# Kernel tuning notes

Hardware: AMD Instinct MI355X
Metric: run time of the kernel (lower is better)

The kernel has to match this reference:

```python
import jax, jax.numpy as jnp
import numpy as np

N = 100000
E = 640000
ND = 128   # node_dim
ED = 128   # edge_dim
HD = 256   # hidden_dim
EPS = 1e-5


def _mlp_ln(x, W1, b1, W2, b2, W3, b3, g, beta):
    h = jax.nn.relu(x @ W1 + b1)
    h = jax.nn.relu(h @ W2 + b2)
    o = h @ W3 + b3
    mu = jnp.mean(o, axis=-1, keepdims=True)
    var = jnp.mean(jnp.square(o - mu), axis=-1, keepdims=True)
    return (o - mu) * jax.lax.rsqrt(var + EPS) * g + beta


def setup_inputs() -> dict:
    key = jax.random.key(0)
    ks = jax.random.split(key, 20)
    s = 0.02
    inp = {
        "node_emb": jax.random.normal(ks[0], (N, ND), jnp.float32),
        "edge_emb": jax.random.normal(ks[1], (E, ED), jnp.float32),
        "src": jax.random.randint(ks[2], (E,), 0, N),
        "dst": jax.random.randint(ks[3], (E,), 0, N),
        "num_nodes": N,
        # edge MLP: in = 2*ND + ED
        "eW1": jax.random.normal(ks[4], (2 * ND + ED, HD), jnp.float32) * s,
        "eb1": jnp.zeros((HD,), jnp.float32),
        "eW2": jax.random.normal(ks[5], (HD, HD), jnp.float32) * s,
        "eb2": jnp.zeros((HD,), jnp.float32),
        "eW3": jax.random.normal(ks[6], (HD, ED), jnp.float32) * s,
        "eb3": jnp.zeros((ED,), jnp.float32),
        "eg": jnp.ones((ED,), jnp.float32),
        "ebeta": jnp.zeros((ED,), jnp.float32),
        # node MLP: in = ND + ED
        "nW1": jax.random.normal(ks[7], (ND + ED, HD), jnp.float32) * s,
        "nb1": jnp.zeros((HD,), jnp.float32),
        "nW2": jax.random.normal(ks[8], (HD, HD), jnp.float32) * s,
        "nb2": jnp.zeros((HD,), jnp.float32),
        "nW3": jax.random.normal(ks[9], (HD, ND), jnp.float32) * s,
        "nb3": jnp.zeros((ND,), jnp.float32),
        "ng": jnp.ones((ND,), jnp.float32),
        "nbeta": jnp.zeros((ND,), jnp.float32),
    }
    return inp


def reference(node_emb, edge_emb, src, dst, num_nodes,
              eW1, eb1, eW2, eb2, eW3, eb3, eg, ebeta,
              nW1, nb1, nW2, nb2, nW3, nb3, ng, nbeta):
    # Edge update: e' = MLP(concat(h_i, h_j, e)) + e
    edge_input = jnp.concatenate([node_emb[src], node_emb[dst], edge_emb], axis=-1)
    edge_emb_new = _mlp_ln(edge_input, eW1, eb1, eW2, eb2, eW3, eb3, eg, ebeta) + edge_emb
    # Mean aggregation over incoming edges per dst node
    agg = jax.ops.segment_sum(edge_emb_new, dst, num_segments=num_nodes)
    count = jax.ops.segment_sum(jnp.ones((dst.shape[0], 1), node_emb.dtype), dst, num_segments=num_nodes)
    agg = agg / jnp.maximum(count, 1.0)
    # Node update: h' = MLP(concat(h, agg)) + h
    node_input = jnp.concatenate([node_emb, agg], axis=-1)
    node_emb_new = _mlp_ln(node_input, nW1, nb1, nW2, nb2, nW3, nb3, ng, nbeta) + node_emb
    return (node_emb_new, edge_emb_new)
```

## Files before the change

### kernel.cpp

```cpp
#include <hip/hip_runtime.h>
#include <hip/hip_bf16.h>

typedef __attribute__((ext_vector_type(8))) short bf16x8;
typedef __attribute__((ext_vector_type(4))) short s16x4;
typedef __attribute__((ext_vector_type(4))) float f32x4;

__device__ __forceinline__ short f2bf(float f) {
  union { __hip_bfloat16 h; short s; } u;
  u.h = __float2bfloat16(f);
  return u.s;
}

__device__ __forceinline__ void gld_lds16(const short* g, short* l) {
  __builtin_amdgcn_global_load_lds((const __attribute__((address_space(1))) unsigned*)g,
                                   (__attribute__((address_space(3))) unsigned*)l,
                                   16, 0, 0);
}

#define BARX(N) asm volatile("s_waitcnt vmcnt(" #N ") lgkmcnt(0)\ns_barrier" ::: "memory")
#define BARLG() asm volatile("s_waitcnt lgkmcnt(0)\ns_barrier" ::: "memory")

template <bool PERM>
__global__ void prep_kernel(const float* __restrict__ W, short* __restrict__ out, int K, int N) {
  int s = blockIdx.x * 256 + threadIdx.x;
  int NF = N >> 4;
  int total = (K >> 5) * NF * 64;
  if (s >= total) return;
  int l = s & 63, kcf = s >> 6;
  int kc = kcf / NF, f = kcf - kc * NF;
  int kg = l >> 4, l16 = l & 15;
  bf16x8 o;
#pragma unroll
  for (int e = 0; e < 8; ++e) {
    int kh = kc * 32 + kg * 8 + e;
    int k = PERM ? ((kh & ~63) | ((kh & 3) << 4) | ((kh >> 2) & 15)) : kh;
    o[e] = f2bf(W[(size_t)k * N + f * 16 + l16]);
  }
  *(bf16x8*)(out + (size_t)s * 8) = o;
}

__global__ void count_kernel(const int* __restrict__ dst, int* __restrict__ cnt, int E) {
  int i = blockIdx.x * 256 + threadIdx.x;
  if (i < E) atomicAdd(&cnt[dst[i]], 1);
}

__global__ __launch_bounds__(1024) void scan_kernel(const int* __restrict__ cnt,
                                                    int* __restrict__ off,
                                                    int* __restrict__ cursor, int N) {
  __shared__ int wsum[16];
  const int t = threadIdx.x;
  const int w = t >> 6, l = t & 63;
  int running = 0;
  for (int base = 0; base < N; base += 1024) {
    int i = base + t;
    int v = (i < N) ? cnt[i] : 0;
    int x = v;
#pragma unroll
    for (int d = 1; d < 64; d <<= 1) { int y = __shfl_up(x, d); if (l >= d) x += y; }
    if (l == 63) wsum[w] = x;
    __syncthreads();
    if (w == 0) {
      int s = (l < 16) ? wsum[l] : 0;
#pragma unroll
      for (int d = 1; d < 16; d <<= 1) { int y = __shfl_up(s, d); if (l >= d) s += y; }
      if (l < 16) wsum[l] = s;
    }
    __syncthreads();
    int total = wsum[15];
    int wo = (w > 0) ? wsum[w - 1] : 0;
    int excl = running + wo + x - v;
    if (i < N) { off[i] = excl; cursor[i] = excl; }
    running += total;
    __syncthreads();
  }
  if (t == 0) off[N] = running;
}

__global__ void scatter_kernel(const int* __restrict__ dst, int* __restrict__ cursor,
                               int* __restrict__ eidx, int E) {
  int e = blockIdx.x * 256 + threadIdx.x;
  if (e < E) {
    int p = atomicAdd(&cursor[dst[e]], 1);
    eidx[p] = e;
  }
}

__global__ void agg_kernel(const float* __restrict__ edge_out, const int* __restrict__ eidx,
                           const int* __restrict__ off, float* __restrict__ agg, int N) {
  int n = blockIdx.x * 4 + (threadIdx.x >> 6);
  if (n >= N) return;
  int l = threadIdx.x & 63;
  int beg = off[n], end = off[n + 1];
  float ax = 0.f, ay = 0.f;
  int i = beg;
  for (; i + 4 <= end; i += 4) {
    int e0 = eidx[i], e1 = eidx[i + 1], e2 = eidx[i + 2], e3 = eidx[i + 3];
    float2 v0 = *(const float2*)(edge_out + (size_t)e0 * 128 + l * 2);
    float2 v1 = *(const float2*)(edge_out + (size_t)e1 * 128 + l * 2);
    float2 v2 = *(const float2*)(edge_out + (size_t)e2 * 128 + l * 2);
    float2 v3 = *(const float2*)(edge_out + (size_t)e3 * 128 + l * 2);
    ax += v0.x + v1.x + v2.x + v3.x;
    ay += v0.y + v1.y + v2.y + v3.y;
  }
  for (; i < end; ++i) {
    int e = eidx[i];
    float2 v = *(const float2*)(edge_out + (size_t)e * 128 + l * 2);
    ax += v.x; ay += v.y;
  }
  float inv = 1.0f / fmaxf((float)(end - beg), 1.0f);
  *(float2*)(agg + (size_t)n * 128 + l * 2) = make_float2(ax * inv, ay * inv);
}

struct F8 { float4 a, b; };

template <bool IS_EDGE>
__launch_bounds__(512, 2)
__global__ void mlp_kernel(const float* __restrict__ node_emb, const float* __restrict__ edge_emb,
                           const int* __restrict__ src, const int* __restrict__ dst,
                           const short* __restrict__ wAll,
                           const float* __restrict__ b1, const float* __restrict__ b2,
                           const float* __restrict__ b3,
                           const float* __restrict__ gam, const float* __restrict__ bet,
                           const float* __restrict__ agg,
                           float* __restrict__ out_base, int M) {
  extern __shared__ short smem[];
  short* BsBase = smem;
  short* AsBase = smem + 24576;
  short* Hs     = smem + 32768;

  const int tid = threadIdx.x;
  const int m0 = blockIdx.x * 128;
  const int w = tid >> 6, lane = tid & 63, l16 = lane & 15, kg = lane >> 4;
  const int wr = w >> 2, wc = w & 3;

  constexpr int NC1 = IS_EDGE ? 12 : 8;

  const int grow = tid >> 2;
  const int gk = tid & 3;
  const int grc = min(m0 + grow, M - 1);
  const int aslot = (grow >> 4) * 64 + gk * 16 + (grow & 15);
  int gsr = 0, gdr = 0;
  if (IS_EDGE) { gsr = src[grc]; gdr = dst[grc]; }

  float b1v[4], b2v[4];
#pragma unroll
  for (int ct = 0; ct < 4; ++ct) {
    int col = wc * 64 + ct * 16 + l16;
    b1v[ct] = b1[col];
    b2v[ct] = b2[col];
  }
  float b3v[8], gv[8], bev[8];
#pragma unroll
  for (int f = 0; f < 8; ++f) {
    int col = f * 16 + l16;
    b3v[f] = b3[col]; gv[f] = gam[col]; bev[f] = bet[col];
  }

  f32x4 acc[16];
#pragma unroll
  for (int i = 0; i < 16; ++i) { f32x4 z = {0.f, 0.f, 0.f, 0.f}; acc[i] = z; }

  auto bsbuf = [&](int v) -> short* { return BsBase + (size_t)(v % 3) * 8192; };
  auto stage1024 = [&](int v) {
    const short* g = wAll + (size_t)v * 8192;
    short* l = bsbuf(v);
    gld_lds16(g + (size_t)tid * 8, l + (size_t)tid * 8);
    gld_lds16(g + (size_t)(512 + tid) * 8, l + (size_t)(512 + tid) * 8);
  };

  auto gatherA = [&](int c) -> F8 {
    const float* q;
    if (IS_EDGE) {
      if (c < 4)      q = node_emb + (size_t)gsr * 128 + c * 32 + gk * 8;
      else if (c < 8) q = node_emb + (size_t)gdr * 128 + (c - 4) * 32 + gk * 8;
      else            q = edge_emb + (size_t)grc * 128 + (c - 8) * 32 + gk * 8;
    } else {
      if (c < 4) q = node_emb + (size_t)grc * 128 + c * 32 + gk * 8;
      else       q = agg + (size_t)grc * 128 + (c - 4) * 32 + gk * 8;
    }
    F8 r;
    r.a = *(const float4*)q;
    r.b = *(const float4*)(q + 4);
    return r;
  };
  auto writeA = [&](const F8& p, int buf) {
    float t[8];
    *(float4*)t = p.a; *(float4*)(t + 4) = p.b;
    bf16x8 o;
#pragma unroll
    for (int e = 0; e < 8; ++e) o[e] = f2bf(t[e]);
    *(bf16x8*)&AsBase[(size_t)buf * 4096 + (size_t)aslot * 8] = o;
  };

  auto mfma16 = [&](bf16x8* a, bf16x8* b) {
#pragma unroll
    for (int rt = 0; rt < 4; ++rt)
#pragma unroll
      for (int ct = 0; ct < 4; ++ct)
        acc[rt * 4 + ct] = __builtin_amdgcn_mfma_f32_16x16x32_bf16(a[rt], b[ct], acc[rt * 4 + ct], 0, 0, 0);
  };

  auto compA = [&](int i) {
    const short* Ap = AsBase + (size_t)(i & 1) * 4096;
    const short* Bp = bsbuf(i);
    bf16x8 a[4], b[4];
#pragma unroll
    for (int rt = 0; rt < 4; ++rt)
      a[rt] = *(const bf16x8*)&Ap[(size_t)((wr * 4 + rt) * 64 + kg * 16 + l16) * 8];
#pragma unroll
    for (int ct = 0; ct < 4; ++ct)
      b[ct] = *(const bf16x8*)&Bp[(size_t)((wc * 4 + ct) * 64 + lane) * 8];
    mfma16(a, b);
  };

  auto computeH = [&](int j, const short* Bp) {
    bf16x8 a[4], b[4];
#pragma unroll
    for (int rt = 0; rt < 4; ++rt) {
      int row = wr * 64 + rt * 16 + l16;
      int ch = (j * 32 + kg * 8) ^ ((row & 7) << 3);
      a[rt] = *(const bf16x8*)&Hs[(size_t)row * 256 + ch];
    }
#pragma unroll
    for (int ct = 0; ct < 4; ++ct)
      b[ct] = *(const bf16x8*)&Bp[(size_t)((wc * 4 + ct) * 64 + lane) * 8];
    mfma16(a, b);
  };

  auto writeH = [&](const float* bv) {
#pragma unroll
    for (int rt = 0; rt < 4; ++rt)
#pragma unroll
      for (int q = 0; q < 4; ++q) {
        int row = wr * 64 + rt * 16 + kg * 4 + q;
        s16x4 v;
#pragma unroll
        for (int ct = 0; ct < 4; ++ct)
          v[ct] = f2bf(fmaxf(acc[rt * 4 + ct][q] + bv[ct], 0.f));
        int ch = (wc * 64 + l16 * 4) ^ ((row & 7) << 3);
        *(s16x4*)&Hs[(size_t)row * 256 + ch] = v;
      }
#pragma unroll
    for (int i = 0; i < 16; ++i) { f32x4 z = {0.f, 0.f, 0.f, 0.f}; acc[i] = z; }
  };

  auto computeL3 = [&](int kk, const short* Bp) {
    int row = w * 16 + l16;
    int ch = (kk * 32 + kg * 8) ^ ((row & 7) << 3);
    bf16x8 a = *(const bf16x8*)&Hs[(size_t)row * 256 + ch];
    const short* Bsub = Bp + (size_t)(kk & 1) * 4096;
#pragma unroll
    for (int f = 0; f < 8; ++f) {
      bf16x8 b = *(const bf16x8*)&Bsub[(size_t)(f * 64 + lane) * 8];
      acc[f] = __builtin_amdgcn_mfma_f32_16x16x32_bf16(a, b, acc[f], 0, 0, 0);
    }
  };

  F8 hold0 = gatherA(0);
  stage1024(0);
  stage1024(1);
  F8 hold = gatherA(1);
  writeA(hold0, 0);
  BARX(4);

#pragma unroll
  for (int i = 0; i < NC1; ++i) {
    stage1024(i + 2);
    F8 gnew = hold;
    if (i + 2 < NC1) gnew = gatherA(i + 2);
    compA(i);
    if (i + 1 < NC1) writeA(hold, (i + 1) & 1);
    if (i + 2 < NC1) { BARX(4); } else { BARX(2); }
    hold = gnew;
  }
  writeH(b1v);
  BARLG();

#pragma unroll
  for (int j = 0; j < 8; ++j) {
    int p = NC1 + j;
    stage1024(p + 2);
    computeH(j, bsbuf(p));
    BARX(2);
  }
  writeH(b2v);
  BARLG();

#pragma unroll
  for (int k = 0; k < 4; ++k) {
    int p = NC1 + 8 + k;
    if (k < 2) stage1024(p + 2);
    computeL3(2 * k, bsbuf(p));
    computeL3(2 * k + 1, bsbuf(p));
    if (k == 0 || k == 1) { BARX(2); }
    else if (k == 2)      { BARX(0); }
  }

#pragma unroll
  for (int q = 0; q < 4; ++q) {
    int rg = m0 + w * 16 + kg * 4 + q;
    float o[8], s1 = 0.f, s2 = 0.f;
#pragma unroll
    for (int f = 0; f < 8; ++f) {
      float x = acc[f][q] + b3v[f];
      o[f] = x; s1 += x; s2 += x * x;
    }
#pragma unroll
    for (int m = 1; m <= 8; m <<= 1) { s1 += __shfl_xor(s1, m); s2 += __shfl_xor(s2, m); }
    float mu = s1 * (1.f / 128.f);
    float var = s2 * (1.f / 128.f) - mu * mu;
    float rs = rsqrtf(var + 1e-5f);
    if (rg < M) {
      const float* resid = (IS_EDGE ? edge_emb : node_emb) + (size_t)rg * 128;
      float* op = out_base + (size_t)rg * 128;
#pragma unroll
      for (int f = 0; f < 8; ++f) {
        int col = f * 16 + l16;
        op[col] = (o[f] - mu) * rs * gv[f] + bev[f] + resid[col];
      }
    }
  }
}

extern "C" void kernel_launch(void* const* d_in, const int* in_sizes, int n_in,
                              void* d_out, int out_size, void* d_ws, size_t ws_size,
                              hipStream_t stream) {
  const float* node_emb = (const float*)d_in[0];
  const float* edge_emb = (const float*)d_in[1];
  const int*   src      = (const int*)d_in[2];
  const int*   dst      = (const int*)d_in[3];
  const float* eW1 = (const float*)d_in[5];
  const float* eb1 = (const float*)d_in[6];
  const float* eW2 = (const float*)d_in[7];
  const float* eb2 = (const float*)d_in[8];
  const float* eW3 = (const float*)d_in[9];
  const float* eb3 = (const float*)d_in[10];
  const float* eg  = (const float*)d_in[11];
  const float* ebt = (const float*)d_in[12];
  const float* nW1 = (const float*)d_in[13];
  const float* nb1 = (const float*)d_in[14];
  const float* nW2 = (const float*)d_in[15];
  const float* nb2 = (const float*)d_in[16];
  const float* nW3 = (const float*)d_in[17];
  const float* nb3 = (const float*)d_in[18];
  const float* ng  = (const float*)d_in[19];
  const float* nbt = (const float*)d_in[20];

  const int Nn = in_sizes[0] / 128;
  const int Ee = in_sizes[2];

  char* ws = (char*)d_ws;
  float* agg  = (float*)ws;  ws += (size_t)Nn * 128 * 4;
  int* cnt_i  = (int*)ws;    ws += (size_t)Nn * 4;
  int* cursor = (int*)ws;    ws += (size_t)Nn * 4;
  int* offv   = (int*)ws;    ws += (size_t)(Nn + 1) * 4;
  int* eidx   = (int*)ws;    ws += (size_t)Ee * 4;
  ws = (char*)(((uintptr_t)ws + 15) & ~(uintptr_t)15);
  short* wp = (short*)ws;
  short* eAll = wp;
  short* nAll = wp + 196608;

  float* out_node = (float*)d_out;
  float* out_edge = out_node + (size_t)Nn * 128;

  hipMemsetAsync(cnt_i, 0, (size_t)Nn * 4, stream);

  prep_kernel<false><<<48, 256, 0, stream>>>(eW1, eAll, 384, 256);
  prep_kernel<true><<<32, 256, 0, stream>>>(eW2, eAll + 98304, 256, 256);
  prep_kernel<true><<<16, 256, 0, stream>>>(eW3, eAll + 163840, 256, 128);
  prep_kernel<false><<<32, 256, 0, stream>>>(nW1, nAll, 256, 256);
  prep_kernel<true><<<32, 256, 0, stream>>>(nW2, nAll + 65536, 256, 256);
  prep_kernel<true><<<16, 256, 0, stream>>>(nW3, nAll + 131072, 256, 128);

  count_kernel<<<(Ee + 255) / 256, 256, 0, stream>>>(dst, cnt_i, Ee);
  scan_kernel<<<1, 1024, 0, stream>>>(cnt_i, offv, cursor, Nn);
  scatter_kernel<<<(Ee + 255) / 256, 256, 0, stream>>>(dst, cursor, eidx, Ee);

  mlp_kernel<true><<<(Ee + 127) / 128, 512, 131072, stream>>>(
      node_emb, edge_emb, src, dst, eAll,
      eb1, eb2, eb3, eg, ebt, agg, out_edge, Ee);

  agg_kernel<<<(Nn + 3) / 4, 256, 0, stream>>>(out_edge, eidx, offv, agg, Nn);

  mlp_kernel<false><<<(Nn + 127) / 128, 512, 131072, stream>>>(
      node_emb, edge_emb, src, dst, nAll,
      nb1, nb2, nb3, ng, nbt, agg, out_node, Nn);
}
```

Baseline: 751.8 us.

## Shrink MLP tiles to 64 rows with 256 threads and double-buffered weights

Reworks the fused MLP kernel from 128-row tiles with 8 waves and triple-buffered weight stages to 64-row tiles with 4 waves and double-buffered weight stages. Each wave now covers all 64 rows and a 64-column slice, shared memory per block drops from 128KB to 72KB, and wait counts are adjusted to fit the new pipeline depth. It also raises wave priority around MFMA bursts and adds scheduling barriers. The aim is more resident blocks and better latency hiding, but weight tiles are reused across half as many rows, so weight loads from L2 double and the shallower prefetch may expose more latency.

```diff
diff --git a/kernel.cpp b/kernel.cpp
--- a/kernel.cpp
+++ b/kernel.cpp
@@ -18,7 +18,6 @@
 }
 
 #define BARX(N) asm volatile("s_waitcnt vmcnt(" #N ") lgkmcnt(0)\ns_barrier" ::: "memory")
-#define BARLG() asm volatile("s_waitcnt lgkmcnt(0)\ns_barrier" ::: "memory")
 
 template <bool PERM>
 __global__ void prep_kernel(const float* __restrict__ W, short* __restrict__ out, int K, int N) {
@@ -114,7 +113,7 @@
 struct F8 { float4 a, b; };
 
 template <bool IS_EDGE>
-__launch_bounds__(512, 2)
+__launch_bounds__(256, 2)
 __global__ void mlp_kernel(const float* __restrict__ node_emb, const float* __restrict__ edge_emb,
                            const int* __restrict__ src, const int* __restrict__ dst,
                            const short* __restrict__ wAll,
@@ -124,14 +123,13 @@
                            const float* __restrict__ agg,
                            float* __restrict__ out_base, int M) {
   extern __shared__ short smem[];
-  short* BsBase = smem;
-  short* AsBase = smem + 24576;
-  short* Hs     = smem + 32768;
+  short* Bs = smem;
+  short* As = smem + 16384;
+  short* Hs = smem + 20480;
 
   const int tid = threadIdx.x;
-  const int m0 = blockIdx.x * 128;
+  const int m0 = blockIdx.x * 64;
   const int w = tid >> 6, lane = tid & 63, l16 = lane & 15, kg = lane >> 4;
-  const int wr = w >> 2, wc = w & 3;
 
   constexpr int NC1 = IS_EDGE ? 12 : 8;
 
@@ -145,7 +143,7 @@
   float b1v[4], b2v[4];
 #pragma unroll
   for (int ct = 0; ct < 4; ++ct) {
-    int col = wc * 64 + ct * 16 + l16;
+    int col = w * 64 + ct * 16 + l16;
     b1v[ct] = b1[col];
     b2v[ct] = b2[col];
   }
@@ -160,12 +158,12 @@
 #pragma unroll
   for (int i = 0; i < 16; ++i) { f32x4 z = {0.f, 0.f, 0.f, 0.f}; acc[i] = z; }
 
-  auto bsbuf = [&](int v) -> short* { return BsBase + (size_t)(v % 3) * 8192; };
-  auto stage1024 = [&](int v) {
+  auto stageU = [&](int v) {
     const short* g = wAll + (size_t)v * 8192;
-    short* l = bsbuf(v);
-    gld_lds16(g + (size_t)tid * 8, l + (size_t)tid * 8);
-    gld_lds16(g + (size_t)(512 + tid) * 8, l + (size_t)(512 + tid) * 8);
+    short* l = Bs + (size_t)(v & 1) * 8192;
+#pragma unroll
+    for (int s0 = 0; s0 < 4; ++s0)
+      gld_lds16(g + (size_t)(s0 * 256 + tid) * 8, l + (size_t)(s0 * 256 + tid) * 8);
   };
 
   auto gatherA = [&](int c) -> F8 {
@@ -189,27 +187,29 @@
     bf16x8 o;
 #pragma unroll
     for (int e = 0; e < 8; ++e) o[e] = f2bf(t[e]);
-    *(bf16x8*)&AsBase[(size_t)buf * 4096 + (size_t)aslot * 8] = o;
+    *(bf16x8*)&As[(size_t)buf * 2048 + (size_t)aslot * 8] = o;
   };
 
   auto mfma16 = [&](bf16x8* a, bf16x8* b) {
+    __builtin_amdgcn_s_setprio(1);
 #pragma unroll
     for (int rt = 0; rt < 4; ++rt)
 #pragma unroll
       for (int ct = 0; ct < 4; ++ct)
         acc[rt * 4 + ct] = __builtin_amdgcn_mfma_f32_16x16x32_bf16(a[rt], b[ct], acc[rt * 4 + ct], 0, 0, 0);
+    __builtin_amdgcn_s_setprio(0);
   };
 
   auto compA = [&](int i) {
-    const short* Ap = AsBase + (size_t)(i & 1) * 4096;
-    const short* Bp = bsbuf(i);
+    const short* Ap = As + (size_t)(i & 1) * 2048;
+    const short* Bp = Bs + (size_t)(i & 1) * 8192;
     bf16x8 a[4], b[4];
 #pragma unroll
     for (int rt = 0; rt < 4; ++rt)
-      a[rt] = *(const bf16x8*)&Ap[(size_t)((wr * 4 + rt) * 64 + kg * 16 + l16) * 8];
+      a[rt] = *(const bf16x8*)&Ap[(size_t)(rt * 64 + kg * 16 + l16) * 8];
 #pragma unroll
     for (int ct = 0; ct < 4; ++ct)
-      b[ct] = *(const bf16x8*)&Bp[(size_t)((wc * 4 + ct) * 64 + lane) * 8];
+      b[ct] = *(const bf16x8*)&Bp[(size_t)((w * 4 + ct) * 64 + lane) * 8];
     mfma16(a, b);
   };
 
@@ -217,13 +217,13 @@
     bf16x8 a[4], b[4];
 #pragma unroll
     for (int rt = 0; rt < 4; ++rt) {
-      int row = wr * 64 + rt * 16 + l16;
+      int row = rt * 16 + l16;
       int ch = (j * 32 + kg * 8) ^ ((row & 7) << 3);
       a[rt] = *(const bf16x8*)&Hs[(size_t)row * 256 + ch];
     }
 #pragma unroll
     for (int ct = 0; ct < 4; ++ct)
-      b[ct] = *(const bf16x8*)&Bp[(size_t)((wc * 4 + ct) * 64 + lane) * 8];
+      b[ct] = *(const bf16x8*)&Bp[(size_t)((w * 4 + ct) * 64 + lane) * 8];
     mfma16(a, b);
   };
 
@@ -232,12 +232,12 @@
     for (int rt = 0; rt < 4; ++rt)
 #pragma unroll
       for (int q = 0; q < 4; ++q) {
-        int row = wr * 64 + rt * 16 + kg * 4 + q;
+        int row = rt * 16 + kg * 4 + q;
         s16x4 v;
 #pragma unroll
         for (int ct = 0; ct < 4; ++ct)
           v[ct] = f2bf(fmaxf(acc[rt * 4 + ct][q] + bv[ct], 0.f));
-        int ch = (wc * 64 + l16 * 4) ^ ((row & 7) << 3);
+        int ch = (w * 64 + l16 * 4) ^ ((row & 7) << 3);
         *(s16x4*)&Hs[(size_t)row * 256 + ch] = v;
       }
 #pragma unroll
@@ -249,51 +249,60 @@
     int ch = (kk * 32 + kg * 8) ^ ((row & 7) << 3);
     bf16x8 a = *(const bf16x8*)&Hs[(size_t)row * 256 + ch];
     const short* Bsub = Bp + (size_t)(kk & 1) * 4096;
+    __builtin_amdgcn_s_setprio(1);
 #pragma unroll
     for (int f = 0; f < 8; ++f) {
       bf16x8 b = *(const bf16x8*)&Bsub[(size_t)(f * 64 + lane) * 8];
       acc[f] = __builtin_amdgcn_mfma_f32_16x16x32_bf16(a, b, acc[f], 0, 0, 0);
     }
-  };
-
-  F8 hold0 = gatherA(0);
-  stage1024(0);
-  stage1024(1);
+    __builtin_amdgcn_s_setprio(0);
+  };
+
+  F8 h0 = gatherA(0);
+  stageU(0);
+  __builtin_amdgcn_sched_barrier(0);
   F8 hold = gatherA(1);
-  writeA(hold0, 0);
-  BARX(4);
+  writeA(h0, 0);
+  __builtin_amdgcn_sched_barrier(0);
+  BARX(2);
 
 #pragma unroll
   for (int i = 0; i < NC1; ++i) {
-    stage1024(i + 2);
+    stageU(i + 1);
+    __builtin_amdgcn_sched_barrier(0);
     F8 gnew = hold;
     if (i + 2 < NC1) gnew = gatherA(i + 2);
+    __builtin_amdgcn_sched_barrier(0);
     compA(i);
     if (i + 1 < NC1) writeA(hold, (i + 1) & 1);
-    if (i + 2 < NC1) { BARX(4); } else { BARX(2); }
+    __builtin_amdgcn_sched_barrier(0);
+    if (i + 2 < NC1)      { BARX(2); }
+    else if (i + 1 < NC1) { BARX(0); }
+    else                  { BARX(4); }
     hold = gnew;
   }
   writeH(b1v);
-  BARLG();
+  BARX(0);
 
 #pragma unroll
   for (int j = 0; j < 8; ++j) {
-    int p = NC1 + j;
-    stage1024(p + 2);
-    computeH(j, bsbuf(p));
-    BARX(2);
+    int u = NC1 + j;
+    stageU(u + 1);
+    computeH(j, Bs + (size_t)(u & 1) * 8192);
+    if (j < 7) { BARX(0); }
+    else       { BARX(4); }
   }
   writeH(b2v);
-  BARLG();
+  BARX(0);
 
 #pragma unroll
   for (int k = 0; k < 4; ++k) {
-    int p = NC1 + 8 + k;
-    if (k < 2) stage1024(p + 2);
-    computeL3(2 * k, bsbuf(p));
-    computeL3(2 * k + 1, bsbuf(p));
-    if (k == 0 || k == 1) { BARX(2); }
-    else if (k == 2)      { BARX(0); }
+    int u = NC1 + 8 + k;
+    if (k < 3) stageU(u + 1);
+    const short* Bp = Bs + (size_t)(u & 1) * 8192;
+    computeL3(2 * k, Bp);
+    computeL3(2 * k + 1, Bp);
+    if (k < 3) { BARX(0); }
   }
 
 #pragma unroll
@@ -376,13 +385,13 @@
   scan_kernel<<<1, 1024, 0, stream>>>(cnt_i, offv, cursor, Nn);
   scatter_kernel<<<(Ee + 255) / 256, 256, 0, stream>>>(dst, cursor, eidx, Ee);
 
-  mlp_kernel<true><<<(Ee + 127) / 128, 512, 131072, stream>>>(
+  mlp_kernel<true><<<(Ee + 63) / 64, 256, 73728, stream>>>(
       node_emb, edge_emb, src, dst, eAll,
       eb1, eb2, eb3, eg, ebt, agg, out_edge, Ee);
 
   agg_kernel<<<(Nn + 3) / 4, 256, 0, stream>>>(out_edge, eidx, offv, agg, Nn);
 
-  mlp_kernel<false><<<(Nn + 127) / 128, 512, 131072, stream>>>(
+  mlp_kernel<false><<<(Nn + 63) / 64, 256, 73728, stream>>>(
       node_emb, edge_emb, src, dst, nAll,
       nb1, nb2, nb3, ng, nbt, agg, out_node, Nn);
 }
```

After: 778.3 us. 1.04x slower.

## Use 1024-thread MLP blocks with smaller per-wave tiles and unified pipeline loop

Applied to the files above, without the earlier changes.

Doubles the MLP kernel block to 16 waves, halving each wave's accumulator tile (2x4 MFMA tiles instead of 4x4) so more waves can hide latency. All three GEMM stages run in one unrolled loop over weight chunks with a single staged load per thread, with sched_barriers and adjusted vmcnt waits. The layer-3 output is split across two column halves, so the LayerNorm statistics are combined through a shared-memory partial-sum buffer and an extra block barrier. B-fragment LDS reads per MFMA go up, and the larger block may lower the number of resident blocks.

```diff
diff --git a/kernel.cpp b/kernel.cpp
--- a/kernel.cpp
+++ b/kernel.cpp
@@ -18,7 +18,6 @@
 }
 
 #define BARX(N) asm volatile("s_waitcnt vmcnt(" #N ") lgkmcnt(0)\ns_barrier" ::: "memory")
-#define BARLG() asm volatile("s_waitcnt lgkmcnt(0)\ns_barrier" ::: "memory")
 
 template <bool PERM>
 __global__ void prep_kernel(const float* __restrict__ W, short* __restrict__ out, int K, int N) {
@@ -111,10 +110,8 @@
   *(float2*)(agg + (size_t)n * 128 + l * 2) = make_float2(ax * inv, ay * inv);
 }
 
-struct F8 { float4 a, b; };
-
 template <bool IS_EDGE>
-__launch_bounds__(512, 2)
+__launch_bounds__(1024, 4)
 __global__ void mlp_kernel(const float* __restrict__ node_emb, const float* __restrict__ edge_emb,
                            const int* __restrict__ src, const int* __restrict__ dst,
                            const short* __restrict__ wAll,
@@ -124,21 +121,24 @@
                            const float* __restrict__ agg,
                            float* __restrict__ out_base, int M) {
   extern __shared__ short smem[];
-  short* BsBase = smem;
-  short* AsBase = smem + 24576;
-  short* Hs     = smem + 32768;
+  short* Bs = smem;
+  short* As = smem + 24576;
+  short* Hs = smem + 32768;
+  float2* pbuf = (float2*)(smem + 24576);
 
   const int tid = threadIdx.x;
   const int m0 = blockIdx.x * 128;
   const int w = tid >> 6, lane = tid & 63, l16 = lane & 15, kg = lane >> 4;
   const int wr = w >> 2, wc = w & 3;
+  const int r8 = w & 7, c2 = w >> 3;
 
   constexpr int NC1 = IS_EDGE ? 12 : 8;
-
-  const int grow = tid >> 2;
-  const int gk = tid & 3;
-  const int grc = min(m0 + grow, M - 1);
-  const int aslot = (grow >> 4) * 64 + gk * 16 + (grow & 15);
+  constexpr int NU = NC1 + 8 + 4;
+
+  const int gr = tid >> 3;
+  const int gq = tid & 7;
+  const int grc = min(m0 + gr, M - 1);
+  const int aoff = ((gr >> 4) * 64 + (gq >> 1) * 16 + (gr & 15)) * 8 + (gq & 1) * 4;
   int gsr = 0, gdr = 0;
   if (IS_EDGE) { gsr = src[grc]; gdr = dst[grc]; }
 
@@ -149,90 +149,76 @@
     b1v[ct] = b1[col];
     b2v[ct] = b2[col];
   }
-  float b3v[8], gv[8], bev[8];
-#pragma unroll
-  for (int f = 0; f < 8; ++f) {
-    int col = f * 16 + l16;
-    b3v[f] = b3[col]; gv[f] = gam[col]; bev[f] = bet[col];
-  }
-
-  f32x4 acc[16];
-#pragma unroll
-  for (int i = 0; i < 16; ++i) { f32x4 z = {0.f, 0.f, 0.f, 0.f}; acc[i] = z; }
-
-  auto bsbuf = [&](int v) -> short* { return BsBase + (size_t)(v % 3) * 8192; };
-  auto stage1024 = [&](int v) {
+
+  f32x4 acc[8];
+#pragma unroll
+  for (int i = 0; i < 8; ++i) { f32x4 z = {0.f, 0.f, 0.f, 0.f}; acc[i] = z; }
+
+  auto stageU = [&](int v) {
     const short* g = wAll + (size_t)v * 8192;
-    short* l = bsbuf(v);
+    short* l = Bs + (size_t)(v % 3) * 8192;
     gld_lds16(g + (size_t)tid * 8, l + (size_t)tid * 8);
-    gld_lds16(g + (size_t)(512 + tid) * 8, l + (size_t)(512 + tid) * 8);
-  };
-
-  auto gatherA = [&](int c) -> F8 {
+  };
+
+  auto gatherA = [&](int c) -> float4 {
+    int co = (c & 3) * 32 + gq * 4;
     const float* q;
     if (IS_EDGE) {
-      if (c < 4)      q = node_emb + (size_t)gsr * 128 + c * 32 + gk * 8;
-      else if (c < 8) q = node_emb + (size_t)gdr * 128 + (c - 4) * 32 + gk * 8;
-      else            q = edge_emb + (size_t)grc * 128 + (c - 8) * 32 + gk * 8;
+      if (c < 4)      q = node_emb + (size_t)gsr * 128 + co;
+      else if (c < 8) q = node_emb + (size_t)gdr * 128 + co;
+      else            q = edge_emb + (size_t)grc * 128 + co;
     } else {
-      if (c < 4) q = node_emb + (size_t)grc * 128 + c * 32 + gk * 8;
-      else       q = agg + (size_t)grc * 128 + (c - 4) * 32 + gk * 8;
-    }
-    F8 r;
-    r.a = *(const float4*)q;
-    r.b = *(const float4*)(q + 4);
-    return r;
-  };
-  auto writeA = [&](const F8& p, int buf) {
-    float t[8];
-    *(float4*)t = p.a; *(float4*)(t + 4) = p.b;
-    bf16x8 o;
-#pragma unroll
-    for (int e = 0; e < 8; ++e) o[e] = f2bf(t[e]);
-    *(bf16x8*)&AsBase[(size_t)buf * 4096 + (size_t)aslot * 8] = o;
-  };
-
-  auto mfma16 = [&](bf16x8* a, bf16x8* b) {
-#pragma unroll
-    for (int rt = 0; rt < 4; ++rt)
+      q = ((c < 4) ? node_emb : agg) + (size_t)grc * 128 + co;
+    }
+    return *(const float4*)q;
+  };
+  auto writeA = [&](float4 p, int buf) {
+    s16x4 o;
+    o[0] = f2bf(p.x); o[1] = f2bf(p.y); o[2] = f2bf(p.z); o[3] = f2bf(p.w);
+    *(s16x4*)&As[(size_t)buf * 4096 + aoff] = o;
+  };
+
+  auto compA = [&](int u) {
+    const short* Ap = As + (size_t)(u & 1) * 4096;
+    const short* Bp = Bs + (size_t)(u % 3) * 8192;
+    bf16x8 a[2], b[4];
+#pragma unroll
+    for (int rt = 0; rt < 2; ++rt)
+      a[rt] = *(const bf16x8*)&Ap[(size_t)((wr * 2 + rt) * 64 + kg * 16 + l16) * 8];
+#pragma unroll
+    for (int ct = 0; ct < 4; ++ct)
+      b[ct] = *(const bf16x8*)&Bp[(size_t)((wc * 4 + ct) * 64 + lane) * 8];
+#pragma unroll
+    for (int rt = 0; rt < 2; ++rt)
 #pragma unroll
       for (int ct = 0; ct < 4; ++ct)
         acc[rt * 4 + ct] = __builtin_amdgcn_mfma_f32_16x16x32_bf16(a[rt], b[ct], acc[rt * 4 + ct], 0, 0, 0);
   };
 
-  auto compA = [&](int i) {
-    const short* Ap = AsBase + (size_t)(i & 1) * 4096;
-    const short* Bp = bsbuf(i);
-    bf16x8 a[4], b[4];
-#pragma unroll
-    for (int rt = 0; rt < 4; ++rt)
-      a[rt] = *(const bf16x8*)&Ap[(size_t)((wr * 4 + rt) * 64 + kg * 16 + l16) * 8];
+  auto computeH = [&](int j, const short* Bp) {
+    bf16x8 a[2], b[4];
+#pragma unroll
+    for (int rt = 0; rt < 2; ++rt) {
+      int row = wr * 32 + rt * 16 + l16;
+      int ch = (j * 32 + kg * 8) ^ ((row & 7) << 3);
+      a[rt] = *(const bf16x8*)&Hs[(size_t)row * 256 + ch];
+    }
 #pragma unroll
     for (int ct = 0; ct < 4; ++ct)
       b[ct] = *(const bf16x8*)&Bp[(size_t)((wc * 4 + ct) * 64 + lane) * 8];
-    mfma16(a, b);
-  };
-
-  auto computeH = [&](int j, const short* Bp) {
-    bf16x8 a[4], b[4];
-#pragma unroll
-    for (int rt = 0; rt < 4; ++rt) {
-      int row = wr * 64 + rt * 16 + l16;
-      int ch = (j * 32 + kg * 8) ^ ((row & 7) << 3);
-      a[rt] = *(const bf16x8*)&Hs[(size_t)row * 256 + ch];
-    }
-#pragma unroll
-    for (int ct = 0; ct < 4; ++ct)
-      b[ct] = *(const bf16x8*)&Bp[(size_t)((wc * 4 + ct) * 64 + lane) * 8];
-    mfma16(a, b);
+#pragma unroll
+    for (int rt = 0; rt < 2; ++rt)
+#pragma unroll
+      for (int ct = 0; ct < 4; ++ct)
+        acc[rt * 4 + ct] = __builtin_amdgcn_mfma_f32_16x16x32_bf16(a[rt], b[ct], acc[rt * 4 + ct], 0, 0, 0);
   };
 
   auto writeH = [&](const float* bv) {
 #pragma unroll
-    for (int rt = 0; rt < 4; ++rt)
+    for (int rt = 0; rt < 2; ++rt)
 #pragma unroll
       for (int q = 0; q < 4; ++q) {
-        int row = wr * 64 + rt * 16 + kg * 4 + q;
+        int row = wr * 32 + rt * 16 + kg * 4 + q;
         s16x4 v;
 #pragma unroll
         for (int ct = 0; ct < 4; ++ct)
@@ -241,82 +227,96 @@
         *(s16x4*)&Hs[(size_t)row * 256 + ch] = v;
       }
 #pragma unroll
-    for (int i = 0; i < 16; ++i) { f32x4 z = {0.f, 0.f, 0.f, 0.f}; acc[i] = z; }
+    for (int i = 0; i < 8; ++i) { f32x4 z = {0.f, 0.f, 0.f, 0.f}; acc[i] = z; }
   };
 
   auto computeL3 = [&](int kk, const short* Bp) {
-    int row = w * 16 + l16;
+    int row = r8 * 16 + l16;
     int ch = (kk * 32 + kg * 8) ^ ((row & 7) << 3);
     bf16x8 a = *(const bf16x8*)&Hs[(size_t)row * 256 + ch];
     const short* Bsub = Bp + (size_t)(kk & 1) * 4096;
 #pragma unroll
-    for (int f = 0; f < 8; ++f) {
-      bf16x8 b = *(const bf16x8*)&Bsub[(size_t)(f * 64 + lane) * 8];
+    for (int f = 0; f < 4; ++f) {
+      bf16x8 b = *(const bf16x8*)&Bsub[(size_t)((c2 * 4 + f) * 64 + lane) * 8];
       acc[f] = __builtin_amdgcn_mfma_f32_16x16x32_bf16(a, b, acc[f], 0, 0, 0);
     }
   };
 
-  F8 hold0 = gatherA(0);
-  stage1024(0);
-  stage1024(1);
-  F8 hold = gatherA(1);
-  writeA(hold0, 0);
-  BARX(4);
-
-#pragma unroll
-  for (int i = 0; i < NC1; ++i) {
-    stage1024(i + 2);
-    F8 gnew = hold;
-    if (i + 2 < NC1) gnew = gatherA(i + 2);
-    compA(i);
-    if (i + 1 < NC1) writeA(hold, (i + 1) & 1);
-    if (i + 2 < NC1) { BARX(4); } else { BARX(2); }
-    hold = gnew;
-  }
-  writeH(b1v);
-  BARLG();
-
-#pragma unroll
-  for (int j = 0; j < 8; ++j) {
-    int p = NC1 + j;
-    stage1024(p + 2);
-    computeH(j, bsbuf(p));
-    BARX(2);
-  }
-  writeH(b2v);
-  BARLG();
-
-#pragma unroll
-  for (int k = 0; k < 4; ++k) {
-    int p = NC1 + 8 + k;
-    if (k < 2) stage1024(p + 2);
-    computeL3(2 * k, bsbuf(p));
-    computeL3(2 * k + 1, bsbuf(p));
-    if (k == 0 || k == 1) { BARX(2); }
-    else if (k == 2)      { BARX(0); }
-  }
-
+  float4 g0 = gatherA(0);
+  float4 ghold = gatherA(1);
+  stageU(0);
+  stageU(1);
+  writeA(g0, 0);
+  BARX(1);
+
+#pragma unroll
+  for (int u = 0; u < NU; ++u) {
+    if (u + 2 < NU) stageU(u + 2);
+    float4 gnew;
+    if (u + 2 < NC1) gnew = gatherA(u + 2);
+    __builtin_amdgcn_sched_barrier(0);
+
+    if (u < NC1) {
+      compA(u);
+    } else if (u < NC1 + 8) {
+      computeH(u - NC1, Bs + (size_t)(u % 3) * 8192);
+    } else {
+      const short* Bp = Bs + (size_t)(u % 3) * 8192;
+      computeL3(2 * (u - NC1 - 8), Bp);
+      computeL3(2 * (u - NC1 - 8) + 1, Bp);
+    }
+    if (u + 1 < NC1) writeA(ghold, (u + 1) & 1);
+    if (u == NC1 - 1) writeH(b1v);
+    if (u == NC1 + 7) {
+      asm volatile("s_waitcnt lgkmcnt(0)\ns_barrier" ::: "memory");
+      writeH(b2v);
+    }
+    __builtin_amdgcn_sched_barrier(0);
+
+    if (u + 2 < NC1)      { BARX(2); }
+    else if (u + 2 < NU)  { BARX(1); }
+    else if (u + 1 < NU)  { BARX(0); }
+    if (u + 2 < NC1) ghold = gnew;
+  }
+
+  float b3v[4], gv[4], bev[4];
+#pragma unroll
+  for (int f = 0; f < 4; ++f) {
+    int col = c2 * 64 + f * 16 + l16;
+    b3v[f] = b3[col]; gv[f] = gam[col]; bev[f] = bet[col];
+  }
 #pragma unroll
   for (int q = 0; q < 4; ++q) {
-    int rg = m0 + w * 16 + kg * 4 + q;
-    float o[8], s1 = 0.f, s2 = 0.f;
-#pragma unroll
-    for (int f = 0; f < 8; ++f) {
+    int row = r8 * 16 + kg * 4 + q;
+    float s1 = 0.f, s2 = 0.f;
+#pragma unroll
+    for (int f = 0; f < 4; ++f) {
       float x = acc[f][q] + b3v[f];
-      o[f] = x; s1 += x; s2 += x * x;
+      acc[f][q] = x;
+      s1 += x; s2 += x * x;
     }
 #pragma unroll
     for (int m = 1; m <= 8; m <<= 1) { s1 += __shfl_xor(s1, m); s2 += __shfl_xor(s2, m); }
-    float mu = s1 * (1.f / 128.f);
-    float var = s2 * (1.f / 128.f) - mu * mu;
+    if (l16 == 0) pbuf[row * 2 + c2] = make_float2(s1, s2);
+  }
+  __syncthreads();
+#pragma unroll
+  for (int q = 0; q < 4; ++q) {
+    int row = r8 * 16 + kg * 4 + q;
+    float2 p0 = pbuf[row * 2];
+    float2 p1 = pbuf[row * 2 + 1];
+    float S1 = p0.x + p1.x, S2 = p0.y + p1.y;
+    float mu = S1 * (1.f / 128.f);
+    float var = S2 * (1.f / 128.f) - mu * mu;
     float rs = rsqrtf(var + 1e-5f);
+    int rg = m0 + row;
     if (rg < M) {
       const float* resid = (IS_EDGE ? edge_emb : node_emb) + (size_t)rg * 128;
       float* op = out_base + (size_t)rg * 128;
 #pragma unroll
-      for (int f = 0; f < 8; ++f) {
-        int col = f * 16 + l16;
-        op[col] = (o[f] - mu) * rs * gv[f] + bev[f] + resid[col];
+      for (int f = 0; f < 4; ++f) {
+        int col = c2 * 64 + f * 16 + l16;
+        op[col] = (acc[f][q] - mu) * rs * gv[f] + bev[f] + resid[col];
       }
     }
   }
@@ -376,13 +376,13 @@
   scan_kernel<<<1, 1024, 0, stream>>>(cnt_i, offv, cursor, Nn);
   scatter_kernel<<<(Ee + 255) / 256, 256, 0, stream>>>(dst, cursor, eidx, Ee);
 
-  mlp_kernel<true><<<(Ee + 127) / 128, 512, 131072, stream>>>(
+  mlp_kernel<true><<<(Ee + 127) / 128, 1024, 131072, stream>>>(
       node_emb, edge_emb, src, dst, eAll,
       eb1, eb2, eb3, eg, ebt, agg, out_edge, Ee);
 
   agg_kernel<<<(Nn + 3) / 4, 256, 0, stream>>>(out_edge, eidx, offv, agg, Nn);
 
-  mlp_kernel<false><<<(Nn + 127) / 128, 512, 131072, stream>>>(
+  mlp_kernel<false><<<(Nn + 127) / 128, 1024, 131072, stream>>>(
       node_emb, edge_emb, src, dst, nAll,
       nb1, nb2, nb3, ng, nbt, agg, out_node, Nn);
 }
```

Result: slower. 850.6 us (+13.1%).

## Precompute per-node first-layer projections and gather them per edge

Applied to the files above, without the earlier changes.

Splits the edge MLP's first layer algebraically. node_emb @ W1[0:128] and node_emb @ W1[128:256] are computed once per node (N rows) in a new pre_kernel and stored as bf16 P/Q buffers. The edge kernel then gathers P[src]+Q[dst] into LDS and adds them to the accumulator, so its first GEMM only covers edge_emb with K=128 instead of 384. This removes two thirds of the layer-1 FLOPs on 640K edges and replaces the two 128-float gathers with two 256-bf16 gathers. It adds an extra kernel plus bf16 rounding of the partial sums, which may change accuracy slightly.

```diff
diff --git a/kernel.cpp b/kernel.cpp
--- a/kernel.cpp
+++ b/kernel.cpp
@@ -9,6 +9,9 @@
   union { __hip_bfloat16 h; short s; } u;
   u.h = __float2bfloat16(f);
   return u.s;
+}
+__device__ __forceinline__ float bf2f(unsigned short s) {
+  union { float f; unsigned u; } v; v.u = ((unsigned)s) << 16; return v.f;
 }
 
 __device__ __forceinline__ void gld_lds16(const short* g, short* l) {
@@ -111,6 +114,99 @@
   *(float2*)(agg + (size_t)n * 128 + l * 2) = make_float2(ax * inv, ay * inv);
 }
 
+__launch_bounds__(512, 2)
+__global__ void pre_kernel(const float* __restrict__ node_emb, const short* __restrict__ wPre,
+                           short* __restrict__ P, short* __restrict__ Q, int Nn) {
+  extern __shared__ short smem[];
+  short* Bs = smem;
+  short* As = smem + 24576;
+  const int tid = threadIdx.x;
+  const int m0 = blockIdx.x * 128;
+  const int w = tid >> 6, lane = tid & 63, l16 = lane & 15, kg = lane >> 4;
+  const int wr = w >> 2, wc = w & 3;
+  const int grow = tid >> 2, gk = tid & 3;
+  const int grc = min(m0 + grow, Nn - 1);
+  const int aslot = (grow >> 4) * 64 + gk * 16 + (grow & 15);
+
+  auto stageU = [&](int v) {
+    const short* g = wPre + (size_t)v * 8192;
+    short* l = Bs + (size_t)(v % 3) * 8192;
+    gld_lds16(g + (size_t)tid * 8, l + (size_t)tid * 8);
+    gld_lds16(g + (size_t)(512 + tid) * 8, l + (size_t)(512 + tid) * 8);
+  };
+
+  float4 ga[4][2];
+#pragma unroll
+  for (int c = 0; c < 4; ++c) {
+    const float* qp = node_emb + (size_t)grc * 128 + c * 32 + gk * 8;
+    ga[c][0] = *(const float4*)qp;
+    ga[c][1] = *(const float4*)(qp + 4);
+  }
+  stageU(0); stageU(1);
+#pragma unroll
+  for (int c = 0; c < 4; ++c) {
+    float t[8];
+    *(float4*)t = ga[c][0]; *(float4*)(t + 4) = ga[c][1];
+    bf16x8 o;
+#pragma unroll
+    for (int e = 0; e < 8; ++e) o[e] = f2bf(t[e]);
+    *(bf16x8*)&As[(size_t)c * 4096 + (size_t)aslot * 8] = o;
+  }
+  BARX(2);
+
+  f32x4 accP[16], accQ[16];
+#pragma unroll
+  for (int i = 0; i < 16; ++i) { f32x4 z = {0.f,0.f,0.f,0.f}; accP[i] = z; accQ[i] = z; }
+
+#pragma unroll
+  for (int u = 0; u < 8; ++u) {
+    if (u + 2 < 8) stageU(u + 2);
+    const short* Ap = As + (size_t)(u & 3) * 4096;
+    const short* Bp = Bs + (size_t)(u % 3) * 8192;
+    bf16x8 a[4], b[4];
+#pragma unroll
+    for (int rt = 0; rt < 4; ++rt)
+      a[rt] = *(const bf16x8*)&Ap[(size_t)((wr * 4 + rt) * 64 + kg * 16 + l16) * 8];
+#pragma unroll
+    for (int ct = 0; ct < 4; ++ct)
+      b[ct] = *(const bf16x8*)&Bp[(size_t)((wc * 4 + ct) * 64 + lane) * 8];
+    if (u < 4) {
+#pragma unroll
+      for (int rt = 0; rt < 4; ++rt)
+#pragma unroll
+        for (int ct = 0; ct < 4; ++ct)
+          accP[rt * 4 + ct] = __builtin_amdgcn_mfma_f32_16x16x32_bf16(a[rt], b[ct], accP[rt * 4 + ct], 0, 0, 0);
+    } else {
+#pragma unroll
+      for (int rt = 0; rt < 4; ++rt)
+#pragma unroll
+        for (int ct = 0; ct < 4; ++ct)
+          accQ[rt * 4 + ct] = __builtin_amdgcn_mfma_f32_16x16x32_bf16(a[rt], b[ct], accQ[rt * 4 + ct], 0, 0, 0);
+    }
+    if (u + 2 < 8)      { BARX(2); }
+    else if (u + 1 < 8) { BARX(0); }
+  }
+
+#pragma unroll
+  for (int rt = 0; rt < 4; ++rt)
+#pragma unroll
+    for (int q = 0; q < 4; ++q) {
+      int row = wr * 64 + rt * 16 + kg * 4 + q;
+      int rg = m0 + row;
+      if (rg < Nn) {
+        s16x4 vp, vq;
+#pragma unroll
+        for (int ct = 0; ct < 4; ++ct) {
+          vp[ct] = f2bf(accP[rt * 4 + ct][q]);
+          vq[ct] = f2bf(accQ[rt * 4 + ct][q]);
+        }
+        size_t base = (size_t)rg * 256 + wc * 64 + l16 * 4;
+        *(s16x4*)&P[base] = vp;
+        *(s16x4*)&Q[base] = vq;
+      }
+    }
+}
+
 struct F8 { float4 a, b; };
 
 template <bool IS_EDGE>
@@ -118,6 +214,7 @@
 __global__ void mlp_kernel(const float* __restrict__ node_emb, const float* __restrict__ edge_emb,
                            const int* __restrict__ src, const int* __restrict__ dst,
                            const short* __restrict__ wAll,
+                           const short* __restrict__ Pbuf, const short* __restrict__ Qbuf,
                            const float* __restrict__ b1, const float* __restrict__ b2,
                            const float* __restrict__ b3,
                            const float* __restrict__ gam, const float* __restrict__ bet,
@@ -133,14 +230,12 @@
   const int w = tid >> 6, lane = tid & 63, l16 = lane & 15, kg = lane >> 4;
   const int wr = w >> 2, wc = w & 3;
 
-  constexpr int NC1 = IS_EDGE ? 12 : 8;
+  constexpr int NC1 = IS_EDGE ? 4 : 8;
 
   const int grow = tid >> 2;
   const int gk = tid & 3;
   const int grc = min(m0 + grow, M - 1);
   const int aslot = (grow >> 4) * 64 + gk * 16 + (grow & 15);
-  int gsr = 0, gdr = 0;
-  if (IS_EDGE) { gsr = src[grc]; gdr = dst[grc]; }
 
   float b1v[4], b2v[4];
 #pragma unroll
@@ -171,12 +266,9 @@
   auto gatherA = [&](int c) -> F8 {
     const float* q;
     if (IS_EDGE) {
-      if (c < 4)      q = node_emb + (size_t)gsr * 128 + c * 32 + gk * 8;
-      else if (c < 8) q = node_emb + (size_t)gdr * 128 + (c - 4) * 32 + gk * 8;
-      else            q = edge_emb + (size_t)grc * 128 + (c - 8) * 32 + gk * 8;
+      q = edge_emb + (size_t)grc * 128 + c * 32 + gk * 8;
     } else {
-      if (c < 4) q = node_emb + (size_t)grc * 128 + c * 32 + gk * 8;
-      else       q = agg + (size_t)grc * 128 + (c - 4) * 32 + gk * 8;
+      q = ((c < 4) ? node_emb : agg) + (size_t)grc * 128 + (c & 3) * 32 + gk * 8;
     }
     F8 r;
     r.a = *(const float4*)q;
@@ -256,12 +348,31 @@
     }
   };
 
-  F8 hold0 = gatherA(0);
+  F8 h0 = gatherA(0);
+  F8 hold = gatherA(1);
   stage1024(0);
   stage1024(1);
-  F8 hold = gatherA(1);
-  writeA(hold0, 0);
-  BARX(4);
+  if (IS_EDGE) {
+    const int r2 = tid >> 2;
+    const int j4 = tid & 3;
+    const int rc2 = min(m0 + r2, M - 1);
+    const int sr = src[rc2], dr = dst[rc2];
+    const short* Pp = Pbuf + (size_t)sr * 256;
+    const short* Qp = Qbuf + (size_t)dr * 256;
+#pragma unroll
+    for (int g = 0; g < 8; ++g) {
+      int pos = j4 * 64 + g * 8;
+      bf16x8 pv = *(const bf16x8*)&Pp[pos];
+      bf16x8 qv = *(const bf16x8*)&Qp[pos];
+      bf16x8 o;
+#pragma unroll
+      for (int e = 0; e < 8; ++e)
+        o[e] = f2bf(bf2f((unsigned short)pv[e]) + bf2f((unsigned short)qv[e]));
+      *(bf16x8*)&Hs[(size_t)r2 * 256 + (pos ^ ((r2 & 7) << 3))] = o;
+    }
+  }
+  writeA(h0, 0);
+  BARX(2);
 
 #pragma unroll
   for (int i = 0; i < NC1; ++i) {
@@ -273,14 +384,29 @@
     if (i + 2 < NC1) { BARX(4); } else { BARX(2); }
     hold = gnew;
   }
+  if (IS_EDGE) {
+#pragma unroll
+    for (int rt = 0; rt < 4; ++rt)
+#pragma unroll
+      for (int q = 0; q < 4; ++q) {
+        int row = wr * 64 + rt * 16 + kg * 4 + q;
+        int base = row * 256;
+        int xo = (row & 7) << 3;
+#pragma unroll
+        for (int ct = 0; ct < 4; ++ct) {
+          int p = wc * 64 + l16 * 4 + ct;
+          acc[rt * 4 + ct][q] += bf2f(*(const unsigned short*)&Hs[base + (p ^ xo)]);
+        }
+      }
+  }
   writeH(b1v);
   BARLG();
 
 #pragma unroll
   for (int j = 0; j < 8; ++j) {
-    int p = NC1 + j;
-    stage1024(p + 2);
-    computeH(j, bsbuf(p));
+    int u = NC1 + j;
+    stage1024(u + 2);
+    computeH(j, bsbuf(u));
     BARX(2);
   }
   writeH(b2v);
@@ -288,10 +414,11 @@
 
 #pragma unroll
   for (int k = 0; k < 4; ++k) {
-    int p = NC1 + 8 + k;
-    if (k < 2) stage1024(p + 2);
-    computeL3(2 * k, bsbuf(p));
-    computeL3(2 * k + 1, bsbuf(p));
+    int u = NC1 + 8 + k;
+    if (k < 2) stage1024(u + 2);
+    const short* Bp = bsbuf(u);
+    computeL3(2 * k, Bp);
+    computeL3(2 * k + 1, Bp);
     if (k == 0 || k == 1) { BARX(2); }
     else if (k == 2)      { BARX(0); }
   }
@@ -356,33 +483,39 @@
   int* offv   = (int*)ws;    ws += (size_t)(Nn + 1) * 4;
   int* eidx   = (int*)ws;    ws += (size_t)Ee * 4;
   ws = (char*)(((uintptr_t)ws + 15) & ~(uintptr_t)15);
-  short* wp = (short*)ws;
-  short* eAll = wp;
-  short* nAll = wp + 196608;
+  short* wPre = (short*)ws;
+  short* eAll = wPre + 65536;
+  short* nAll = eAll + 131072;
+  short* Pbuf = nAll + 163840;
+  short* Qbuf = Pbuf + (size_t)Nn * 256;
 
   float* out_node = (float*)d_out;
   float* out_edge = out_node + (size_t)Nn * 128;
 
   hipMemsetAsync(cnt_i, 0, (size_t)Nn * 4, stream);
 
-  prep_kernel<false><<<48, 256, 0, stream>>>(eW1, eAll, 384, 256);
-  prep_kernel<true><<<32, 256, 0, stream>>>(eW2, eAll + 98304, 256, 256);
-  prep_kernel<true><<<16, 256, 0, stream>>>(eW3, eAll + 163840, 256, 128);
+  prep_kernel<false><<<16, 256, 0, stream>>>(eW1, wPre, 128, 256);
+  prep_kernel<false><<<16, 256, 0, stream>>>(eW1 + 128 * 256, wPre + 32768, 128, 256);
+  prep_kernel<false><<<16, 256, 0, stream>>>(eW1 + 256 * 256, eAll, 128, 256);
+  prep_kernel<true><<<32, 256, 0, stream>>>(eW2, eAll + 32768, 256, 256);
+  prep_kernel<true><<<16, 256, 0, stream>>>(eW3, eAll + 98304, 256, 128);
   prep_kernel<false><<<32, 256, 0, stream>>>(nW1, nAll, 256, 256);
   prep_kernel<true><<<32, 256, 0, stream>>>(nW2, nAll + 65536, 256, 256);
   prep_kernel<true><<<16, 256, 0, stream>>>(nW3, nAll + 131072, 256, 128);
 
+  pre_kernel<<<(Nn + 127) / 128, 512, 81920, stream>>>(node_emb, wPre, Pbuf, Qbuf, Nn);
+
   count_kernel<<<(Ee + 255) / 256, 256, 0, stream>>>(dst, cnt_i, Ee);
   scan_kernel<<<1, 1024, 0, stream>>>(cnt_i, offv, cursor, Nn);
   scatter_kernel<<<(Ee + 255) / 256, 256, 0, stream>>>(dst, cursor, eidx, Ee);
 
   mlp_kernel<true><<<(Ee + 127) / 128, 512, 131072, stream>>>(
-      node_emb, edge_emb, src, dst, eAll,
+      node_emb, edge_emb, src, dst, eAll, Pbuf, Qbuf,
       eb1, eb2, eb3, eg, ebt, agg, out_edge, Ee);
 
   agg_kernel<<<(Nn + 3) / 4, 256, 0, stream>>>(out_edge, eidx, offv, agg, Nn);
 
   mlp_kernel<false><<<(Nn + 127) / 128, 512, 131072, stream>>>(
-      node_emb, edge_emb, src, dst, nAll,
+      node_emb, edge_emb, src, dst, nAll, Pbuf, Qbuf,
       nb1, nb2, nb3, ng, nbt, agg, out_node, Nn);
 }
```

Result: slower. 901.4 us (+19.9%).
